# Optimization experiments

Hardware: AMD Instinct MI355X
Metric: run time of the kernel (lower is better)

Reference implementation:

```python
import jax, jax.numpy as jnp
import numpy as np

N_NODES = 100000
N_EDGES = 1600000
IN_C = 128
OUT_C = 128


def setup_inputs() -> dict:
    key = jax.random.key(0)
    k1, k2, k3, k4 = jax.random.split(key, 4)
    x = jax.random.normal(k1, (N_NODES, IN_C), dtype=jnp.float32)
    W = jax.random.normal(k2, (IN_C, OUT_C), dtype=jnp.float32) * (1.0 / np.sqrt(IN_C))
    b = jax.random.normal(k3, (OUT_C,), dtype=jnp.float32) * 0.02
    edge_index = jax.random.randint(k4, (2, N_EDGES), 0, N_NODES, dtype=jnp.int32)
    return {"x": x, "W": W, "b": b, "edge_index": edge_index}


def reference(x, W, b, edge_index):
    N = x.shape[0]
    # Symmetrize edges: concat(edge_index, flip(edge_index)) as in adj()
    row = jnp.concatenate([edge_index[0], edge_index[1]])  # [2E]
    col = jnp.concatenate([edge_index[1], edge_index[0]])  # [2E]
    w = jnp.ones(row.shape, dtype=x.dtype)
    # gcn_norm with self loops (fill value 1): deg includes self-loop weight
    deg = jax.ops.segment_sum(w, row, num_segments=N) + 1.0
    dinv = jnp.where(deg > 0, jax.lax.rsqrt(deg), 0.0)  # [N]
    # Dense linear projection (bias=False)
    xw = x @ W  # [N, out]
    # SpMM: y[row] += dinv[row]*dinv[col] * xw[col]  (scatter-add == coalesced adj matmul)
    norm = dinv[row] * dinv[col]  # [2E]
    msgs = norm[:, None] * xw[col]  # [2E, out] -- dominant memory traffic
    y = jax.ops.segment_sum(msgs, row, num_segments=N)
    # Self-loop contribution: weight dinv[i]^2
    y = y + (dinv * dinv)[:, None] * xw
    return y + b
```

## Files before the change

kernel.cpp:

```cpp
#include <hip/hip_runtime.h>
#include <math.h>

constexpr int N = 100000;
constexpr int E = 1600000;
constexpr int C = 128;
constexpr int NPB   = 256;
constexpr int NBUCK = (N + NPB - 1) / NPB;
constexpr int CAP   = 9472;

__device__ inline unsigned f2bf(float f) {
    unsigned u = __float_as_uint(f);
    return (u + 0x7fffu + ((u >> 16) & 1u)) >> 16;
}
__device__ inline unsigned pack2(float lo, float hi) {
    return f2bf(lo) | (f2bf(hi) << 16);
}
__device__ inline float bf_lo(unsigned m) { return __uint_as_float(m << 16); }
__device__ inline float bf_hi(unsigned m) { return __uint_as_float(m & 0xffff0000u); }

__global__ __launch_bounds__(256) void k_bin(const int* __restrict__ ei,
                                             int* __restrict__ gcount,
                                             unsigned* __restrict__ staging) {
    __shared__ int cnt[NBUCK];
    __shared__ int wbase[NBUCK];
    const int t = threadIdx.x;
    const long tile = (long)blockIdx.x * 2048;
    for (int i = t; i < NBUCK; i += 256) cnt[i] = 0;
    __syncthreads();
    int b0[8], b1[8], lo0[8], lo1[8];
    unsigned p0[8], p1[8];
    bool val[8];
#pragma unroll
    for (int j = 0; j < 8; ++j) {
        long e = tile + j * 256 + t;
        val[j] = e < E;
        if (val[j]) {
            int u = __builtin_nontemporal_load(ei + e);
            int v = __builtin_nontemporal_load(ei + E + e);
            b0[j] = u >> 8;
            b1[j] = v >> 8;
            p0[j] = ((unsigned)(u & 255) << 17) | (unsigned)v;
            p1[j] = ((unsigned)(v & 255) << 17) | (unsigned)u;
            lo0[j] = atomicAdd(&cnt[b0[j]], 1);
            lo1[j] = atomicAdd(&cnt[b1[j]], 1);
        }
    }
    __syncthreads();
    for (int i = t; i < NBUCK; i += 256) wbase[i] = atomicAdd(&gcount[i], cnt[i]);
    __syncthreads();
#pragma unroll
    for (int j = 0; j < 8; ++j) {
        if (val[j]) {
            staging[(size_t)b0[j] * CAP + wbase[b0[j]] + lo0[j]] = p0[j];
            staging[(size_t)b1[j] * CAP + wbase[b1[j]] + lo1[j]] = p1[j];
        }
    }
}

__global__ __launch_bounds__(512) void k_csr(const unsigned* __restrict__ staging,
                                             const int* __restrict__ gcount,
                                             int* __restrict__ deg,
                                             float* __restrict__ dinv,
                                             int* __restrict__ rowptr,
                                             int* __restrict__ adj) {
    __shared__ int hist[NPB + 1];
    __shared__ int wpart[8];
    __shared__ int wsum[8];
    __shared__ int sh_base;
    const int g = blockIdx.x;
    const int t = threadIdx.x;
    const int lane = t & 63, wid = t >> 6;
    const int cnt = gcount[g];
    int s = (t < g) ? gcount[t] : 0;
#pragma unroll
    for (int off = 32; off; off >>= 1) s += __shfl_down(s, off);
    if (lane == 0) wsum[wid] = s;
    for (int i = t; i <= NPB; i += 512) hist[i] = 0;
    __syncthreads();
    if (t == 0) {
        int r = 0;
#pragma unroll
        for (int w = 0; w < 8; ++w) r += wsum[w];
        sh_base = r;
    }
    const unsigned* base = staging + (size_t)g * CAP;
    for (int i = t; i < cnt; i += 512) atomicAdd(&hist[base[i] >> 17], 1);
    __syncthreads();
    const int a = (t < NPB) ? hist[t] : 0;
    int v = a;
#pragma unroll
    for (int off = 1; off < 64; off <<= 1) {
        int n = __shfl_up(v, off);
        if (lane >= off) v += n;
    }
    if (lane == 63 && wid < NPB / 64) wpart[wid] = v;
    __syncthreads();
    if (t == 0) {
        int r = 0;
#pragma unroll
        for (int w = 0; w < NPB / 64; ++w) { int x = wpart[w]; wpart[w] = r; r += x; }
    }
    __syncthreads();
    if (t < NPB) hist[t] = v - a + wpart[wid];
    if (t == 0) hist[NPB] = cnt;
    __syncthreads();
    const int nbase = g * NPB;
    const int nlocal = min(NPB, N - nbase);
    const int bbase = sh_base;
    if (t < nlocal) {
        const int st = hist[t], en = hist[t + 1];
        const int d = en - st;
        deg[nbase + t] = d;
        dinv[nbase + t] = rsqrtf((float)d + 1.0f);
        rowptr[nbase + t] = bbase + st;
    }
    __syncthreads();
    int* aslice = adj + bbase;
    for (int i = t; i < cnt; i += 512) {
        const unsigned e = base[i];
        const int pos = atomicAdd(&hist[e >> 17], 1);
        aslice[pos] = (int)(e & 0x1ffffu);
    }
}

__global__ __launch_bounds__(256) void k_gemm(const float* __restrict__ x,
                                              const float* __restrict__ W,
                                              const float* __restrict__ dinv,
                                              unsigned* __restrict__ z16) {
    __shared__ float Ws[32][128];
    __shared__ float xs[64][33];

    const int t   = threadIdx.x;
    const int r0  = (t & 15) * 4;
    const int c0  = (t >> 4) * 8;
    const int bid = blockIdx.x;

    float acc[4][8];
#pragma unroll
    for (int i = 0; i < 4; ++i)
#pragma unroll
        for (int j = 0; j < 8; ++j) acc[i][j] = 0.0f;

    const int lrow = t >> 2;
    const int lk   = (t & 3) * 8;
    const long grow = (long)bid * 64 + lrow;
    const bool rvalid = grow < N;

    for (int k0 = 0; k0 < C; k0 += 32) {
        const float4* Wg = (const float4*)(W + (size_t)k0 * C);
        float4* Wsv = (float4*)(&Ws[0][0]);
#pragma unroll
        for (int j = 0; j < 4; ++j) Wsv[t + 256 * j] = Wg[t + 256 * j];
        float4 a0 = {0, 0, 0, 0}, a1 = {0, 0, 0, 0};
        if (rvalid) {
            a0 = *(const float4*)(x + grow * C + k0 + lk);
            a1 = *(const float4*)(x + grow * C + k0 + lk + 4);
        }
        xs[lrow][lk + 0] = a0.x; xs[lrow][lk + 1] = a0.y;
        xs[lrow][lk + 2] = a0.z; xs[lrow][lk + 3] = a0.w;
        xs[lrow][lk + 4] = a1.x; xs[lrow][lk + 5] = a1.y;
        xs[lrow][lk + 6] = a1.z; xs[lrow][lk + 7] = a1.w;
        __syncthreads();

#pragma unroll 8
        for (int k = 0; k < 32; ++k) {
            float4 w0 = *(const float4*)&Ws[k][c0];
            float4 w1 = *(const float4*)&Ws[k][c0 + 4];
            float xv[4];
#pragma unroll
            for (int i = 0; i < 4; ++i) xv[i] = xs[r0 + i][k];
#pragma unroll
            for (int i = 0; i < 4; ++i) {
                acc[i][0] = fmaf(xv[i], w0.x, acc[i][0]);
                acc[i][1] = fmaf(xv[i], w0.y, acc[i][1]);
                acc[i][2] = fmaf(xv[i], w0.z, acc[i][2]);
                acc[i][3] = fmaf(xv[i], w0.w, acc[i][3]);
                acc[i][4] = fmaf(xv[i], w1.x, acc[i][4]);
                acc[i][5] = fmaf(xv[i], w1.y, acc[i][5]);
                acc[i][6] = fmaf(xv[i], w1.z, acc[i][6]);
                acc[i][7] = fmaf(xv[i], w1.w, acc[i][7]);
            }
        }
        __syncthreads();
    }

#pragma unroll
    for (int i = 0; i < 4; ++i) {
        long r = (long)bid * 64 + r0 + i;
        if (r >= N) break;
        const float dv = dinv[r];
        uint4 pk = {pack2(dv * acc[i][0], dv * acc[i][1]), pack2(dv * acc[i][2], dv * acc[i][3]),
                    pack2(dv * acc[i][4], dv * acc[i][5]), pack2(dv * acc[i][6], dv * acc[i][7])};
        *(uint4*)(z16 + r * (C / 2) + (c0 >> 1)) = pk;
    }
}

__global__ __launch_bounds__(256) void k_gather(const int* __restrict__ rowptr,
                                                const int* __restrict__ deg,
                                                const float* __restrict__ dinv,
                                                const int* __restrict__ adj,
                                                const unsigned* __restrict__ z16,
                                                const float* __restrict__ b,
                                                float* __restrict__ out) {
    const int u = blockIdx.x * 4 + (threadIdx.x >> 6);
    if (u >= N) return;
    const int lane = threadIdx.x & 63;
    const int d  = __builtin_amdgcn_readfirstlane(deg[u]);
    const int st = __builtin_amdgcn_readfirstlane(rowptr[u]);
    const float du = dinv[u];
    const unsigned ms = z16[((unsigned)u << 6) + lane];
    float ax0 = bf_lo(ms), ay0 = bf_hi(ms);
    float ax1 = 0.f, ay1 = 0.f;

    for (int j0 = 0; j0 < d; j0 += 64) {
        int v = 0;
        if (j0 + lane < d) v = adj[st + j0 + lane];
        const int cntc = min(64, d - j0);
        int jj = 0;
        for (; jj + 8 <= cntc; jj += 8) {
            const int v0 = __builtin_amdgcn_readlane(v, jj + 0);
            const int v1 = __builtin_amdgcn_readlane(v, jj + 1);
            const int v2 = __builtin_amdgcn_readlane(v, jj + 2);
            const int v3 = __builtin_amdgcn_readlane(v, jj + 3);
            const int v4 = __builtin_amdgcn_readlane(v, jj + 4);
            const int v5 = __builtin_amdgcn_readlane(v, jj + 5);
            const int v6 = __builtin_amdgcn_readlane(v, jj + 6);
            const int v7 = __builtin_amdgcn_readlane(v, jj + 7);
            const unsigned m0 = (z16 + (((size_t)(unsigned)v0) << 6))[lane];
            const unsigned m1 = (z16 + (((size_t)(unsigned)v1) << 6))[lane];
            const unsigned m2 = (z16 + (((size_t)(unsigned)v2) << 6))[lane];
            const unsigned m3 = (z16 + (((size_t)(unsigned)v3) << 6))[lane];
            const unsigned m4 = (z16 + (((size_t)(unsigned)v4) << 6))[lane];
            const unsigned m5 = (z16 + (((size_t)(unsigned)v5) << 6))[lane];
            const unsigned m6 = (z16 + (((size_t)(unsigned)v6) << 6))[lane];
            const unsigned m7 = (z16 + (((size_t)(unsigned)v7) << 6))[lane];
            ax0 += bf_lo(m0); ay0 += bf_hi(m0);
            ax1 += bf_lo(m1); ay1 += bf_hi(m1);
            ax0 += bf_lo(m2); ay0 += bf_hi(m2);
            ax1 += bf_lo(m3); ay1 += bf_hi(m3);
            ax0 += bf_lo(m4); ay0 += bf_hi(m4);
            ax1 += bf_lo(m5); ay1 += bf_hi(m5);
            ax0 += bf_lo(m6); ay0 += bf_hi(m6);
            ax1 += bf_lo(m7); ay1 += bf_hi(m7);
        }
        for (; jj < cntc; ++jj) {
            const int vv = __builtin_amdgcn_readlane(v, jj);
            const unsigned m = (z16 + (((size_t)(unsigned)vv) << 6))[lane];
            ax0 += bf_lo(m); ay0 += bf_hi(m);
        }
    }
    const float2 bb = *(const float2*)(b + 2 * lane);
    const float ax = ax0 + ax1, ay = ay0 + ay1;
    float2 o = {fmaf(du, ax, bb.x), fmaf(du, ay, bb.y)};
    *(float2*)(out + (size_t)u * C + 2 * lane) = o;
}

extern "C" void kernel_launch(void* const* d_in, const int* in_sizes, int n_in,
                              void* d_out, int out_size, void* d_ws, size_t ws_size,
                              hipStream_t stream) {
    const float* x  = (const float*)d_in[0];
    const float* W  = (const float*)d_in[1];
    const float* b  = (const float*)d_in[2];
    const int*   ei = (const int*)d_in[3];
    float* out = (float*)d_out;

    char* p = (char*)d_ws;
    unsigned* z16 = (unsigned*)p;   p += (size_t)N * (C / 2) * sizeof(unsigned);
    int* deg = (int*)p;             p += (size_t)N * sizeof(int);
    float* dinv = (float*)p;        p += (size_t)N * sizeof(float);
    int* rowptr = (int*)p;          p += (size_t)(N + 4) * sizeof(int);
    int* gcount = (int*)p;          p += 512 * sizeof(int);
    unsigned* staging = (unsigned*)p; p += (size_t)NBUCK * CAP * sizeof(unsigned);
    int* adj = (int*)p;

    hipMemsetAsync(gcount, 0, 512 * sizeof(int), stream);
    k_bin<<<(E + 2047) / 2048, 256, 0, stream>>>(ei, gcount, staging);
    k_csr<<<NBUCK, 512, 0, stream>>>(staging, gcount, deg, dinv, rowptr, adj);
    k_gemm<<<(N + 63) / 64, 256, 0, stream>>>(x, W, dinv, z16);
    k_gather<<<(N + 3) / 4, 256, 0, stream>>>(rowptr, deg, dinv, adj, z16, b, out);
}
```

Before: 324.6 us.

## Split wavefront into four edge groups with 16-byte neighbor row loads

The gather kernel now splits each 64-lane wavefront into four 16-lane quarters. Each quarter loads a whole neighbor row with uint4 (16-byte) loads, so four edges are processed per instruction instead of one edge per 4-byte-per-lane load. Full 64-edge chunks issue 16 loads, with the first eight kept in flight while the rest are accumulated. Partial sums are reduced across the quarters with xor shuffles, and only one quarter writes float4 outputs. This cuts the number of load instructions and serial edge iterations, at the cost of extra registers and a cross-lane reduction per node.

Result: slower. 369.1 us (+13.7%).

```diff
diff --git a/kernel.cpp b/kernel.cpp
--- a/kernel.cpp
+++ b/kernel.cpp
@@ -205,54 +205,79 @@
     const int u = blockIdx.x * 4 + (threadIdx.x >> 6);
     if (u >= N) return;
     const int lane = threadIdx.x & 63;
+    const int q    = lane >> 4;
+    const int c    = lane & 15;
     const int d  = __builtin_amdgcn_readfirstlane(deg[u]);
     const int st = __builtin_amdgcn_readfirstlane(rowptr[u]);
     const float du = dinv[u];
-    const unsigned ms = z16[((unsigned)u << 6) + lane];
-    float ax0 = bf_lo(ms), ay0 = bf_hi(ms);
-    float ax1 = 0.f, ay1 = 0.f;
+
+    float acc[8];
+#pragma unroll
+    for (int i = 0; i < 8; ++i) acc[i] = 0.f;
+
+#define LDG(g) (*(const uint4*)(z16 + (((size_t)(unsigned)__shfl(v, 4 * (g) + q)) << 6) + 4 * c))
+#define ACC(m)                                            \
+    {                                                     \
+        acc[0] += bf_lo((m).x); acc[1] += bf_hi((m).x);   \
+        acc[2] += bf_lo((m).y); acc[3] += bf_hi((m).y);   \
+        acc[4] += bf_lo((m).z); acc[5] += bf_hi((m).z);   \
+        acc[6] += bf_lo((m).w); acc[7] += bf_hi((m).w);   \
+    }
+
+    if (q == 0) {
+        uint4 m = *(const uint4*)(z16 + ((size_t)(unsigned)u << 6) + 4 * c);
+        ACC(m);
+    }
 
     for (int j0 = 0; j0 < d; j0 += 64) {
+        const int cntc = min(64, d - j0);
         int v = 0;
-        if (j0 + lane < d) v = adj[st + j0 + lane];
-        const int cntc = min(64, d - j0);
-        int jj = 0;
-        for (; jj + 8 <= cntc; jj += 8) {
-            const int v0 = __builtin_amdgcn_readlane(v, jj + 0);
-            const int v1 = __builtin_amdgcn_readlane(v, jj + 1);
-            const int v2 = __builtin_amdgcn_readlane(v, jj + 2);
-            const int v3 = __builtin_amdgcn_readlane(v, jj + 3);
-            const int v4 = __builtin_amdgcn_readlane(v, jj + 4);
-            const int v5 = __builtin_amdgcn_readlane(v, jj + 5);
-            const int v6 = __builtin_amdgcn_readlane(v, jj + 6);
-            const int v7 = __builtin_amdgcn_readlane(v, jj + 7);
-            const unsigned m0 = (z16 + (((size_t)(unsigned)v0) << 6))[lane];
-            const unsigned m1 = (z16 + (((size_t)(unsigned)v1) << 6))[lane];
-            const unsigned m2 = (z16 + (((size_t)(unsigned)v2) << 6))[lane];
-            const unsigned m3 = (z16 + (((size_t)(unsigned)v3) << 6))[lane];
-            const unsigned m4 = (z16 + (((size_t)(unsigned)v4) << 6))[lane];
-            const unsigned m5 = (z16 + (((size_t)(unsigned)v5) << 6))[lane];
-            const unsigned m6 = (z16 + (((size_t)(unsigned)v6) << 6))[lane];
-            const unsigned m7 = (z16 + (((size_t)(unsigned)v7) << 6))[lane];
-            ax0 += bf_lo(m0); ay0 += bf_hi(m0);
-            ax1 += bf_lo(m1); ay1 += bf_hi(m1);
-            ax0 += bf_lo(m2); ay0 += bf_hi(m2);
-            ax1 += bf_lo(m3); ay1 += bf_hi(m3);
-            ax0 += bf_lo(m4); ay0 += bf_hi(m4);
-            ax1 += bf_lo(m5); ay1 += bf_hi(m5);
-            ax0 += bf_lo(m6); ay0 += bf_hi(m6);
-            ax1 += bf_lo(m7); ay1 += bf_hi(m7);
-        }
-        for (; jj < cntc; ++jj) {
-            const int vv = __builtin_amdgcn_readlane(v, jj);
-            const unsigned m = (z16 + (((size_t)(unsigned)vv) << 6))[lane];
-            ax0 += bf_lo(m); ay0 += bf_hi(m);
-        }
-    }
-    const float2 bb = *(const float2*)(b + 2 * lane);
-    const float ax = ax0 + ax1, ay = ay0 + ay1;
-    float2 o = {fmaf(du, ax, bb.x), fmaf(du, ay, bb.y)};
-    *(float2*)(out + (size_t)u * C + 2 * lane) = o;
+        if (lane < cntc) v = adj[st + j0 + lane];
+        if (cntc == 64) {
+            uint4 m0 = LDG(0), m1 = LDG(1), m2 = LDG(2), m3 = LDG(3);
+            uint4 m4 = LDG(4), m5 = LDG(5), m6 = LDG(6), m7 = LDG(7);
+            uint4 n0 = LDG(8);  ACC(m0);
+            uint4 n1 = LDG(9);  ACC(m1);
+            uint4 n2 = LDG(10); ACC(m2);
+            uint4 n3 = LDG(11); ACC(m3);
+            uint4 n4 = LDG(12); ACC(m4);
+            uint4 n5 = LDG(13); ACC(m5);
+            uint4 n6 = LDG(14); ACC(m6);
+            uint4 n7 = LDG(15); ACC(m7);
+            ACC(n0); ACC(n1); ACC(n2); ACC(n3);
+            ACC(n4); ACC(n5); ACC(n6); ACC(n7);
+        } else {
+            const int ng = (cntc + 3) >> 2;
+            for (int g = 0; g < ng; ++g) {
+                const int e = 4 * g + q;
+                const int vq = __shfl(v, e);
+                if (e < cntc) {
+                    uint4 m = *(const uint4*)(z16 + (((size_t)(unsigned)vq) << 6) + 4 * c);
+                    ACC(m);
+                }
+            }
+        }
+    }
+#undef LDG
+#undef ACC
+
+#pragma unroll
+    for (int i = 0; i < 8; ++i) {
+        acc[i] += __shfl_xor(acc[i], 16);
+        acc[i] += __shfl_xor(acc[i], 32);
+    }
+
+    if (q == 0) {
+        const float4 b0 = *(const float4*)(b + 8 * c);
+        const float4 b1 = *(const float4*)(b + 8 * c + 4);
+        float4 o0, o1;
+        o0.x = fmaf(du, acc[0], b0.x); o0.y = fmaf(du, acc[1], b0.y);
+        o0.z = fmaf(du, acc[2], b0.z); o0.w = fmaf(du, acc[3], b0.w);
+        o1.x = fmaf(du, acc[4], b1.x); o1.y = fmaf(du, acc[5], b1.y);
+        o1.z = fmaf(du, acc[6], b1.z); o1.w = fmaf(du, acc[7], b1.w);
+        *(float4*)(out + (size_t)u * C + 8 * c)     = o0;
+        *(float4*)(out + (size_t)u * C + 8 * c + 4) = o1;
+    }
 }
 
 extern "C" void kernel_launch(void* const* d_in, const int* in_sizes, int n_in,
```

## Split bf16 features into column halves and pad adjacency for paired-edge gathers

Applied to the files above, without the earlier changes.

Stores the projected features as two separate 64-column halves, and launches the gather kernel twice over so each block handles one half. Within a wave, each half-wave loads a different neighbour, so one load instruction fetches two edges' rows. Adjacency lists are now padded to multiples of 8 with a sentinel zero row, and each bucket gets a fixed-stride slice, which removes the global prefix sum and the remainder loop. Staging memory is reused as the feature buffer. This costs an extra fill of the padded adjacency, padding waste of up to seven dummy loads per node, and a cross-half shuffle reduction.

Result: slower. 333.1 us (+2.6%).

```diff
diff --git a/kernel.cpp b/kernel.cpp
--- a/kernel.cpp
+++ b/kernel.cpp
@@ -7,6 +7,7 @@
 constexpr int NPB   = 256;
 constexpr int NBUCK = (N + NPB - 1) / NPB;
 constexpr int CAP   = 9472;
+constexpr int ADJ_STRIDE = CAP + NPB * 7;
 
 __device__ inline unsigned f2bf(float f) {
     unsigned u = __float_as_uint(f);
@@ -63,70 +64,62 @@
                                              float* __restrict__ dinv,
                                              int* __restrict__ rowptr,
                                              int* __restrict__ adj) {
-    __shared__ int hist[NPB + 1];
-    __shared__ int wpart[8];
-    __shared__ int wsum[8];
-    __shared__ int sh_base;
+    __shared__ int hist[NPB];
+    __shared__ int wpart[4];
     const int g = blockIdx.x;
     const int t = threadIdx.x;
     const int lane = t & 63, wid = t >> 6;
     const int cnt = gcount[g];
-    int s = (t < g) ? gcount[t] : 0;
-#pragma unroll
-    for (int off = 32; off; off >>= 1) s += __shfl_down(s, off);
-    if (lane == 0) wsum[wid] = s;
-    for (int i = t; i <= NPB; i += 512) hist[i] = 0;
-    __syncthreads();
-    if (t == 0) {
-        int r = 0;
-#pragma unroll
-        for (int w = 0; w < 8; ++w) r += wsum[w];
-        sh_base = r;
-    }
+    int* slice = adj + (size_t)g * ADJ_STRIDE;
+    {
+        const int4 fill = {N, N, N, N};
+        for (int i = t; i < ADJ_STRIDE / 4; i += 512) ((int4*)slice)[i] = fill;
+    }
+    for (int i = t; i < NPB; i += 512) hist[i] = 0;
+    __syncthreads();
     const unsigned* base = staging + (size_t)g * CAP;
     for (int i = t; i < cnt; i += 512) atomicAdd(&hist[base[i] >> 17], 1);
     __syncthreads();
-    const int a = (t < NPB) ? hist[t] : 0;
-    int v = a;
+    const int d  = (t < NPB) ? hist[t] : 0;
+    const int pd = (d + 7) & ~7;
+    int v = pd;
 #pragma unroll
     for (int off = 1; off < 64; off <<= 1) {
         int n = __shfl_up(v, off);
         if (lane >= off) v += n;
     }
-    if (lane == 63 && wid < NPB / 64) wpart[wid] = v;
+    if (lane == 63 && wid < 4) wpart[wid] = v;
     __syncthreads();
     if (t == 0) {
         int r = 0;
 #pragma unroll
-        for (int w = 0; w < NPB / 64; ++w) { int x = wpart[w]; wpart[w] = r; r += x; }
-    }
-    __syncthreads();
-    if (t < NPB) hist[t] = v - a + wpart[wid];
-    if (t == 0) hist[NPB] = cnt;
-    __syncthreads();
-    const int nbase = g * NPB;
-    const int nlocal = min(NPB, N - nbase);
-    const int bbase = sh_base;
-    if (t < nlocal) {
-        const int st = hist[t], en = hist[t + 1];
-        const int d = en - st;
-        deg[nbase + t] = d;
-        dinv[nbase + t] = rsqrtf((float)d + 1.0f);
-        rowptr[nbase + t] = bbase + st;
-    }
-    __syncthreads();
-    int* aslice = adj + bbase;
+        for (int w = 0; w < 4; ++w) { int x = wpart[w]; wpart[w] = r; r += x; }
+    }
+    __syncthreads();
+    const int pstart = v - pd + ((wid < 4) ? wpart[wid] : 0);
+    if (t < NPB) {
+        const int node = g * NPB + t;
+        if (node < N) {
+            deg[node]    = d;
+            dinv[node]   = rsqrtf((float)d + 1.0f);
+            rowptr[node] = g * ADJ_STRIDE + pstart;
+        }
+    }
+    __syncthreads();
+    if (t < NPB) hist[t] = pstart;
+    __syncthreads();
     for (int i = t; i < cnt; i += 512) {
         const unsigned e = base[i];
         const int pos = atomicAdd(&hist[e >> 17], 1);
-        aslice[pos] = (int)(e & 0x1ffffu);
+        slice[pos] = (int)(e & 0x1ffffu);
     }
 }
 
 __global__ __launch_bounds__(256) void k_gemm(const float* __restrict__ x,
                                               const float* __restrict__ W,
                                               const float* __restrict__ dinv,
-                                              unsigned* __restrict__ z16) {
+                                              unsigned* __restrict__ z_lo,
+                                              unsigned* __restrict__ z_hi) {
     __shared__ float Ws[32][128];
     __shared__ float xs[64][33];
 
@@ -184,6 +177,8 @@
         __syncthreads();
     }
 
+    unsigned* zh = (c0 < 64) ? z_lo : z_hi;
+    const int ch = (c0 & 63) >> 1;
 #pragma unroll
     for (int i = 0; i < 4; ++i) {
         long r = (long)bid * 64 + r0 + i;
@@ -191,7 +186,7 @@
         const float dv = dinv[r];
         uint4 pk = {pack2(dv * acc[i][0], dv * acc[i][1]), pack2(dv * acc[i][2], dv * acc[i][3]),
                     pack2(dv * acc[i][4], dv * acc[i][5]), pack2(dv * acc[i][6], dv * acc[i][7])};
-        *(uint4*)(z16 + r * (C / 2) + (c0 >> 1)) = pk;
+        *(uint4*)(zh + r * 32 + ch) = pk;
     }
 }
 
@@ -199,60 +194,59 @@
                                                 const int* __restrict__ deg,
                                                 const float* __restrict__ dinv,
                                                 const int* __restrict__ adj,
-                                                const unsigned* __restrict__ z16,
+                                                const unsigned* __restrict__ z_lo,
+                                                const unsigned* __restrict__ z_hi,
                                                 const float* __restrict__ b,
-                                                float* __restrict__ out) {
-    const int u = blockIdx.x * 4 + (threadIdx.x >> 6);
+                                                float* __restrict__ out,
+                                                int nb_h) {
+    const int half = (blockIdx.x >= nb_h) ? 1 : 0;
+    const int u = (blockIdx.x - half * nb_h) * 4 + (threadIdx.x >> 6);
     if (u >= N) return;
     const int lane = threadIdx.x & 63;
+    const int h = lane >> 5;
+    const int c = lane & 31;
     const int d  = __builtin_amdgcn_readfirstlane(deg[u]);
+    const int pd = (d + 7) & ~7;
     const int st = __builtin_amdgcn_readfirstlane(rowptr[u]);
     const float du = dinv[u];
-    const unsigned ms = z16[((unsigned)u << 6) + lane];
-    float ax0 = bf_lo(ms), ay0 = bf_hi(ms);
-    float ax1 = 0.f, ay1 = 0.f;
-
-    for (int j0 = 0; j0 < d; j0 += 64) {
+    const unsigned* zh = (half ? z_hi : z_lo) + c;
+
+    float ax, ay;
+    {
+        const unsigned ms = (h == 0) ? zh[(size_t)(unsigned)u << 5] : 0u;
+        ax = bf_lo(ms); ay = bf_hi(ms);
+    }
+
+#define RL(i) __builtin_amdgcn_readlane(v, (i))
+#define LDP(P) (zh[(size_t)(unsigned)(h ? RL(2 * (P) + 1) : RL(2 * (P))) << 5])
+#define ACC(m) { ax += bf_lo(m); ay += bf_hi(m); }
+
+    for (int j0 = 0; j0 < pd; j0 += 64) {
+        const int cntc = min(64, pd - j0);
         int v = 0;
-        if (j0 + lane < d) v = adj[st + j0 + lane];
-        const int cntc = min(64, d - j0);
-        int jj = 0;
-        for (; jj + 8 <= cntc; jj += 8) {
-            const int v0 = __builtin_amdgcn_readlane(v, jj + 0);
-            const int v1 = __builtin_amdgcn_readlane(v, jj + 1);
-            const int v2 = __builtin_amdgcn_readlane(v, jj + 2);
-            const int v3 = __builtin_amdgcn_readlane(v, jj + 3);
-            const int v4 = __builtin_amdgcn_readlane(v, jj + 4);
-            const int v5 = __builtin_amdgcn_readlane(v, jj + 5);
-            const int v6 = __builtin_amdgcn_readlane(v, jj + 6);
-            const int v7 = __builtin_amdgcn_readlane(v, jj + 7);
-            const unsigned m0 = (z16 + (((size_t)(unsigned)v0) << 6))[lane];
-            const unsigned m1 = (z16 + (((size_t)(unsigned)v1) << 6))[lane];
-            const unsigned m2 = (z16 + (((size_t)(unsigned)v2) << 6))[lane];
-            const unsigned m3 = (z16 + (((size_t)(unsigned)v3) << 6))[lane];
-            const unsigned m4 = (z16 + (((size_t)(unsigned)v4) << 6))[lane];
-            const unsigned m5 = (z16 + (((size_t)(unsigned)v5) << 6))[lane];
-            const unsigned m6 = (z16 + (((size_t)(unsigned)v6) << 6))[lane];
-            const unsigned m7 = (z16 + (((size_t)(unsigned)v7) << 6))[lane];
-            ax0 += bf_lo(m0); ay0 += bf_hi(m0);
-            ax1 += bf_lo(m1); ay1 += bf_hi(m1);
-            ax0 += bf_lo(m2); ay0 += bf_hi(m2);
-            ax1 += bf_lo(m3); ay1 += bf_hi(m3);
-            ax0 += bf_lo(m4); ay0 += bf_hi(m4);
-            ax1 += bf_lo(m5); ay1 += bf_hi(m5);
-            ax0 += bf_lo(m6); ay0 += bf_hi(m6);
-            ax1 += bf_lo(m7); ay1 += bf_hi(m7);
-        }
-        for (; jj < cntc; ++jj) {
-            const int vv = __builtin_amdgcn_readlane(v, jj);
-            const unsigned m = (z16 + (((size_t)(unsigned)vv) << 6))[lane];
-            ax0 += bf_lo(m); ay0 += bf_hi(m);
-        }
-    }
-    const float2 bb = *(const float2*)(b + 2 * lane);
-    const float ax = ax0 + ax1, ay = ay0 + ay1;
-    float2 o = {fmaf(du, ax, bb.x), fmaf(du, ay, bb.y)};
-    *(float2*)(out + (size_t)u * C + 2 * lane) = o;
+        if (lane < cntc) v = adj[st + j0 + lane];
+        const int np = cntc >> 1;
+        unsigned m0 = LDP(0), m1 = LDP(1), m2 = LDP(2), m3 = LDP(3);
+        for (int p = 4; p < np; p += 4) {
+            unsigned n0 = LDP(p), n1 = LDP(p + 1), n2 = LDP(p + 2), n3 = LDP(p + 3);
+            ACC(m0); ACC(m1); ACC(m2); ACC(m3);
+            m0 = n0; m1 = n1; m2 = n2; m3 = n3;
+        }
+        ACC(m0); ACC(m1); ACC(m2); ACC(m3);
+    }
+#undef RL
+#undef LDP
+#undef ACC
+
+    ax += __shfl_xor(ax, 32);
+    ay += __shfl_xor(ay, 32);
+
+    if (h == 0) {
+        const float* bh = b + 64 * half + 2 * c;
+        const float2 bb = {bh[0], bh[1]};
+        float2 o = {fmaf(du, ax, bb.x), fmaf(du, ay, bb.y)};
+        *(float2*)(out + (size_t)u * C + 64 * half + 2 * c) = o;
+    }
 }
 
 extern "C" void kernel_launch(void* const* d_in, const int* in_sizes, int n_in,
@@ -265,17 +259,23 @@
     float* out = (float*)d_out;
 
     char* p = (char*)d_ws;
-    unsigned* z16 = (unsigned*)p;   p += (size_t)N * (C / 2) * sizeof(unsigned);
+    unsigned* zbase = (unsigned*)p;
+    unsigned* z_lo = zbase;
+    unsigned* z_hi = zbase + (size_t)(N + 1) * 32;
+    unsigned* staging = zbase;
+    p += (size_t)2 * (N + 1) * 32 * sizeof(unsigned);
+    int* adj = (int*)p;             p += (size_t)NBUCK * ADJ_STRIDE * sizeof(int);
     int* deg = (int*)p;             p += (size_t)N * sizeof(int);
     float* dinv = (float*)p;        p += (size_t)N * sizeof(float);
     int* rowptr = (int*)p;          p += (size_t)(N + 4) * sizeof(int);
     int* gcount = (int*)p;          p += 512 * sizeof(int);
-    unsigned* staging = (unsigned*)p; p += (size_t)NBUCK * CAP * sizeof(unsigned);
-    int* adj = (int*)p;
 
     hipMemsetAsync(gcount, 0, 512 * sizeof(int), stream);
     k_bin<<<(E + 2047) / 2048, 256, 0, stream>>>(ei, gcount, staging);
     k_csr<<<NBUCK, 512, 0, stream>>>(staging, gcount, deg, dinv, rowptr, adj);
-    k_gemm<<<(N + 63) / 64, 256, 0, stream>>>(x, W, dinv, z16);
-    k_gather<<<(N + 3) / 4, 256, 0, stream>>>(rowptr, deg, dinv, adj, z16, b, out);
-}
+    hipMemsetAsync(z_lo + (size_t)N * 32, 0, 128, stream);
+    hipMemsetAsync(z_hi + (size_t)N * 32, 0, 128, stream);
+    k_gemm<<<(N + 63) / 64, 256, 0, stream>>>(x, W, dinv, z_lo, z_hi);
+    const int nb_h = (N + 3) / 4;
+    k_gather<<<2 * nb_h, 256, 0, stream>>>(rowptr, deg, dinv, adj, z_lo, z_hi, b, out, nb_h);
+}
```
